# Optimization experiments

Measured on AMD Instinct MI355X. Metric: run time of the kernel, lower is better.

## Reference

```python
import jax, jax.numpy as jnp
import numpy as np

NUM_EMBEDDINGS = 4096
EMBED_DIM = 256
BETA = 0.25


def setup_inputs() -> dict:
    key = jax.random.key(0)
    kz, ke = jax.random.split(key)
    z = jax.random.normal(kz, (16, 4096, EMBED_DIM), dtype=jnp.float32)
    lim = 1.0 / NUM_EMBEDDINGS
    emb = jax.random.uniform(ke, (NUM_EMBEDDINGS, EMBED_DIM), dtype=jnp.float32,
                             minval=-lim, maxval=lim)
    return {"z": z, "emb": emb}


def reference(z, emb):
    B, T, D = z.shape
    flat_z = z.reshape(-1, D)                                  # [N, D]
    # squared euclidean distances via ||z||^2 - 2 z.e^T + ||e||^2
    dist = (jnp.sum(flat_z ** 2, axis=1, keepdims=True)
            - 2.0 * flat_z @ emb.T
            + jnp.sum(emb ** 2, axis=1))                       # [N, K]
    indices = jnp.argmin(dist, axis=1)                         # [N]
    z_q = emb[indices].reshape(z.shape)                        # [B, T, D]
    sg = jax.lax.stop_gradient
    codebook_loss = jnp.mean((sg(z_q) - z) ** 2)
    commit_loss = jnp.mean((z_q - sg(z)) ** 2)
    loss = codebook_loss + BETA * commit_loss
    z_q_st = z + sg(z_q - z)                                   # straight-through
    return z_q_st, loss, indices.reshape(B, T)
```

## Files before the change

### kernel.cpp

```cpp
#include <hip/hip_runtime.h>

#define N_ROWS 65536
#define K_CODES 4096
#define D_DIM 256
#define MARGIN_BF 6.0e-5f
#define CAP_DUEL 24576
#define CAP_FULL 8192

typedef __attribute__((ext_vector_type(8))) _Float16 f16x8;
typedef __attribute__((ext_vector_type(4))) float f32x4;

typedef __attribute__((address_space(1))) unsigned int g_u32;
typedef __attribute__((address_space(3))) unsigned int l_u32;
#define GLOAD16(gp, lp) __builtin_amdgcn_global_load_lds((g_u32*)(gp), (l_u32*)(lp), 16, 0, 0)


union f16u { _Float16 h; unsigned short u; };

static __device__ __forceinline__ unsigned int pack2(float a, float b) {
    f16u x, y; x.h = (_Float16)a; y.h = (_Float16)b;
    return (unsigned)x.u | ((unsigned)y.u << 16);
}

static __device__ __forceinline__ void norm_body(const float* __restrict__ src,
                                                 float* __restrict__ dst, int bi, int tid) {
    int row = bi * 64 + (tid >> 2);
    int q = tid & 3;
    const float* p = src + (size_t)row * D_DIM;
    double acc = 0.0;
#pragma unroll 4
    for (int it = 0; it < 16; ++it) {
        float4 v = *(const float4*)&p[(q + 4 * it) * 4];
        float a = v.x * v.x, b = v.y * v.y, c = v.z * v.z, d = v.w * v.w;
        acc += (double)a; acc += (double)b; acc += (double)c; acc += (double)d;
    }
    acc += __shfl_xor(acc, 1);
    acc += __shfl_xor(acc, 2);
    if (q == 0) dst[row] = (float)acc;
}

__global__ __launch_bounds__(256) void cvt_emb_kernel(const float* __restrict__ emb,
                                                      unsigned short* __restrict__ emb_perm,
                                                      float* __restrict__ cvec,
                                                      int* __restrict__ cnts,
                                                      unsigned long long* __restrict__ rescored) {
    if (blockIdx.x >= 512) {
        if (blockIdx.x == 512 && threadIdx.x < 2) cnts[threadIdx.x] = 0;
        norm_body(emb, cvec, blockIdx.x - 512, threadIdx.x);
        return;
    }
    if (blockIdx.x < 256) rescored[blockIdx.x * 256 + threadIdx.x] = ~0ull;
    int gid = blockIdx.x * 256 + threadIdx.x;
    int lane = gid & 63;
    int f = gid >> 6;
    int cf = f & 1;
    int d8 = (f >> 1) & 7;
    int step = (f >> 4) & 63;
    int h = f >> 10;
    int code = h * 2048 + step * 32 + cf * 16 + (lane & 15);
    int d0 = d8 * 32 + (lane >> 4) * 8;
    const float* p = emb + (size_t)code * D_DIM + d0;
    float4 v0 = *(const float4*)p;
    float4 v1 = *(const float4*)(p + 4);
    uint4 o;
    o.x = pack2(v0.x * 4096.0f, v0.y * 4096.0f);
    o.y = pack2(v0.z * 4096.0f, v0.w * 4096.0f);
    o.z = pack2(v1.x * 4096.0f, v1.y * 4096.0f);
    o.w = pack2(v1.z * 4096.0f, v1.w * 4096.0f);
    *(uint4*)((char*)emb_perm + (size_t)gid * 16) = o;
}

__global__ __launch_bounds__(256) void cvt_z_kernel(const float* __restrict__ z,
                                                    unsigned short* __restrict__ z_perm) {
    int ft = blockIdx.x * 256 + threadIdx.x;
    int lane = ft & 63;
    int rf = (ft >> 6) & 3;
    int d8 = (ft >> 8) & 7;
    int rg = ft >> 11;
    int row = rg * 64 + rf * 16 + (lane & 15);
    int d0 = d8 * 32 + (lane >> 4) * 8;
    const float* p = z + (size_t)row * D_DIM + d0;
    float4 v0 = *(const float4*)p;
    float4 v1 = *(const float4*)(p + 4);
    uint4 o;
    o.x = pack2(v0.x, v0.y);
    o.y = pack2(v0.z, v0.w);
    o.z = pack2(v1.x, v1.y);
    o.w = pack2(v1.z, v1.w);
    *(uint4*)((char*)z_perm + (size_t)ft * 16) = o;
}

__global__ __launch_bounds__(256, 2) void phaseB_kernel(
        const unsigned short* __restrict__ z_perm, const unsigned short* __restrict__ emb_perm,
        const float* __restrict__ cvec, float* __restrict__ out_idx,
        int* __restrict__ cnts, int* __restrict__ fulllist,
        unsigned long long* __restrict__ duellist) {
    __shared__ float cv[4096];
    __shared__ unsigned short ring[2][8][1024];

    const int tid = threadIdx.x;
    const int lane = tid & 63;
    const int w = tid >> 6;
    const int pp = w >> 1;
    const int h = w & 1;
    const int l15 = lane & 15, l4 = lane >> 4;
    const int rb = blockIdx.x;

#pragma unroll
    for (int i = 0; i < 4; ++i) {
        int idx = i * 1024 + tid * 4;
        *(float4*)&cv[idx] = *(const float4*)&cvec[idx];
    }

    f16x8 A[8][4];
    {
        const char* zsrc = (const char*)z_perm + (size_t)(rb * 2 + pp) * 32768 + lane * 16;
#pragma unroll
        for (int d8 = 0; d8 < 8; ++d8)
#pragma unroll
            for (int rf = 0; rf < 4; ++rf)
                A[d8][rf] = *(const f16x8*)(zsrc + (d8 * 4 + rf) * 1024);
    }
    __syncthreads();

    const char* bsrc = (const char*)emb_perm + (size_t)h * 1048576 + pp * 1024 + lane * 16;
    char* ldst = (char*)&ring[h][0][0] + pp * 1024;
    const char* lrd = (const char*)&ring[h][0][0] + lane * 16;

#pragma unroll
    for (int q = 0; q < 6; ++q)
        GLOAD16(bsrc + q * 2048, ldst + q * 2048);
    asm volatile("s_waitcnt vmcnt(5)" ::: "memory");
    __builtin_amdgcn_s_barrier();
    __builtin_amdgcn_sched_barrier(0);

    f16x8 B0a = *(const f16x8*)(lrd);
    f16x8 B0b = *(const f16x8*)(lrd + 1024);
    f16x8 B1a, B1b;

    float m1[16], m2[16], m3[16];
#pragma unroll
    for (int t = 0; t < 16; ++t) { m1[t] = 3.4e38f; m2[t] = 3.4e38f; m3[t] = 3.4e38f; }

    f32x4 acc[4][2];

    for (int step = 0; step < 64; ++step) {
        const int kb = h * 2048 + step * 32;
        float ck0 = cv[kb + l15];
        float ck1 = cv[kb + 16 + l15];
#pragma unroll
        for (int rf = 0; rf < 4; ++rf) {
            acc[rf][0] = (f32x4){0.f, 0.f, 0.f, 0.f};
            acc[rf][1] = (f32x4){0.f, 0.f, 0.f, 0.f};
        }
#pragma unroll
        for (int d8 = 0; d8 < 8; ++d8) {
            {
                const char* g = bsrc + (size_t)(step * 8 + d8 + 6) * 2048
                                - ((step == 63 && d8 >= 2) ? 1048576 : 0);
                GLOAD16(g, ldst + ((d8 + 6) & 7) * 2048);
            }
            asm volatile("s_waitcnt vmcnt(5)" ::: "memory");
            __builtin_amdgcn_s_barrier();
            __builtin_amdgcn_sched_barrier(0);
            {
                const char* rp = lrd + ((d8 + 1) & 7) * 2048;
                if ((d8 + 1) & 1) { B1a = *(const f16x8*)rp; B1b = *(const f16x8*)(rp + 1024); }
                else              { B0a = *(const f16x8*)rp; B0b = *(const f16x8*)(rp + 1024); }
            }
            f16x8 b0 = (d8 & 1) ? B1a : B0a;
            f16x8 b1 = (d8 & 1) ? B1b : B0b;
#pragma unroll
            for (int rf = 0; rf < 4; ++rf) {
                acc[rf][0] = __builtin_amdgcn_mfma_f32_16x16x32_f16(A[d8][rf], b0, acc[rf][0], 0, 0, 0);
                acc[rf][1] = __builtin_amdgcn_mfma_f32_16x16x32_f16(A[d8][rf], b1, acc[rf][1], 0, 0, 0);
            }
        }

#pragma unroll
        for (int cf = 0; cf < 2; ++cf) {
            const float ck = cf ? ck1 : ck0;
            const unsigned cg = (unsigned)(kb + cf * 16 + l15);
#pragma unroll
            for (int rf = 0; rf < 4; ++rf)
#pragma unroll
                for (int j = 0; j < 4; ++j) {
                    float d = fmaf(-4.8828125e-4f, acc[rf][cf][j], ck);
                    float dp = __uint_as_float((__float_as_uint(d) & 0xfffff000u) | cg);
                    const int t = rf * 4 + j;
                    m3[t] = __builtin_amdgcn_fmed3f(dp, m2[t], m3[t]);
                    m2[t] = __builtin_amdgcn_fmed3f(dp, m1[t], m2[t]);
                    m1[t] = fminf(m1[t], dp);
                }
        }
    }

    __syncthreads();
    float* m1s = cv;
    float* m2s = cv + 256;
    float* m3s = cv + 512;
#pragma unroll
    for (int t = 0; t < 16; ++t) {
        float a1 = m1[t], a2 = m2[t], a3 = m3[t];
        for (int msk = 8; msk >= 1; msk >>= 1) {
            float b1 = __shfl_xor(a1, msk);
            float b2 = __shfl_xor(a2, msk);
            float b3 = __shfl_xor(a3, msk);
            bool bw = b1 < a1;
            float w1 = bw ? b1 : a1, w2 = bw ? b2 : a2, w3 = bw ? b3 : a3;
            float l1 = bw ? a1 : b1, l2 = bw ? a2 : b2;
            bool t2 = l1 < w2;
            a1 = w1;
            a2 = t2 ? l1 : w2;
            a3 = t2 ? fminf(w2, l2) : fminf(w3, l1);
        }
        if (l15 == 0) {
            int rloc = (t >> 2) * 16 + l4 * 4 + (t & 3);
            m1s[w * 64 + rloc] = a1;
            m2s[w * 64 + rloc] = a2;
            m3s[w * 64 + rloc] = a3;
        }
    }
    __syncthreads();

    if (tid < 128) {
        int pg = tid >> 6, r = tid & 63;
        int wA = pg * 2, wB = pg * 2 + 1;
        float a1 = m1s[wA * 64 + r], a2 = m2s[wA * 64 + r], a3 = m3s[wA * 64 + r];
        float b1 = m1s[wB * 64 + r], b2 = m2s[wB * 64 + r], b3 = m3s[wB * 64 + r];
        bool bw = b1 < a1;
        float w1 = bw ? b1 : a1, w2 = bw ? b2 : a2, w3 = bw ? b3 : a3;
        float l1 = bw ? a1 : b1, l2 = bw ? a2 : b2;
        bool t2 = l1 < w2;
        float f1 = w1;
        float f2 = t2 ? l1 : w2;
        float f3 = t2 ? fminf(w2, l2) : fminf(w3, l1);

        int i1 = (int)(__float_as_uint(f1) & 0xfffu);
        int i2 = (int)(__float_as_uint(f2) & 0xfffu);
        int rowg = rb * 128 + pg * 64 + r;
        out_idx[rowg] = (float)i1;
        if (f3 - f1 < MARGIN_BF) {
            int pz = atomicAdd(&cnts[1], 1);
            if (pz < CAP_FULL) fulllist[pz] = rowg;
        } else if (f2 - f1 < MARGIN_BF) {
            int pz = atomicAdd(&cnts[0], 1);
            if (pz < CAP_DUEL) {
                duellist[pz] = ((unsigned long long)(unsigned)rowg << 32) |
                               ((unsigned)i1 << 16) | (unsigned)i2;
            } else {
                int pf = atomicAdd(&cnts[1], 1);
                if (pf < CAP_FULL) fulllist[pf] = rowg;
            }
        }
    }
}

__global__ __launch_bounds__(256) void duel_kernel(
        const float* __restrict__ z, const float* __restrict__ emb,
        const float* __restrict__ cvec,
        const int* __restrict__ cnts, const unsigned long long* __restrict__ duellist,
        unsigned long long* __restrict__ rescored) {
    int n = cnts[0];
    if (n > CAP_DUEL) n = CAP_DUEL;
    for (int i = blockIdx.x * 256 + threadIdx.x; i < n; i += 64 * 256) {
        unsigned long long e = duellist[i];
        int row = (int)(e >> 32);
        int c1 = (int)((e >> 16) & 0xfffu);
        int c2 = (int)(e & 0xfffu);
        const float* zp = z + (size_t)row * D_DIM;
        const float* p1 = emb + (size_t)c1 * D_DIM;
        const float* p2 = emb + (size_t)c2 * D_DIM;
        float a1 = 0.f, a2 = 0.f;
        double n0 = 0.0, n1 = 0.0, n2 = 0.0, n3 = 0.0;
#pragma unroll 8
        for (int d4 = 0; d4 < 64; ++d4) {
            float4 zf = *(const float4*)&zp[d4 * 4];
            float4 e1 = *(const float4*)&p1[d4 * 4];
            float4 e2 = *(const float4*)&p2[d4 * 4];
            a1 = fmaf(zf.x, e1.x, a1); a1 = fmaf(zf.y, e1.y, a1);
            a1 = fmaf(zf.z, e1.z, a1); a1 = fmaf(zf.w, e1.w, a1);
            a2 = fmaf(zf.x, e2.x, a2); a2 = fmaf(zf.y, e2.y, a2);
            a2 = fmaf(zf.z, e2.z, a2); a2 = fmaf(zf.w, e2.w, a2);
            float sx = zf.x * zf.x, sy = zf.y * zf.y, sz = zf.z * zf.z, sw = zf.w * zf.w;
            switch (d4 & 3) {
                case 0: n0 += (double)sx; n0 += (double)sy; n0 += (double)sz; n0 += (double)sw; break;
                case 1: n1 += (double)sx; n1 += (double)sy; n1 += (double)sz; n1 += (double)sw; break;
                case 2: n2 += (double)sx; n2 += (double)sy; n2 += (double)sz; n2 += (double)sw; break;
                default: n3 += (double)sx; n3 += (double)sy; n3 += (double)sz; n3 += (double)sw; break;
            }
        }
        float rn = (float)((n0 + n1) + (n2 + n3));
        float d1 = __fadd_rn(__fsub_rn(rn, __fmul_rn(2.0f, a1)), cvec[c1]);
        float d2 = __fadd_rn(__fsub_rn(rn, __fmul_rn(2.0f, a2)), cvec[c2]);
        unsigned long long p1v = ((unsigned long long)__float_as_uint(d1) << 32) | (unsigned)c1;
        unsigned long long p2v = ((unsigned long long)__float_as_uint(d2) << 32) | (unsigned)c2;
        rescored[row] = p1v < p2v ? p1v : p2v;
    }
}

__global__ __launch_bounds__(256) void rescore_kernel(
        const float* __restrict__ z, const float* __restrict__ emb,
        const float* __restrict__ cvec,
        const int* __restrict__ cnts, const int* __restrict__ fulllist,
        unsigned long long* __restrict__ rescored) {
    __shared__ float zs[16][256];
    __shared__ float sa[16];
    __shared__ int srow[16];
    const int tid = threadIdx.x;
    int cnt = cnts[1];
    if (cnt > CAP_FULL) cnt = CAP_FULL;
    const int nu = ((cnt + 15) >> 4) << 2;
    for (int uu = blockIdx.x; uu < nu; uu += gridDim.x) {
        int rg = uu >> 2, ks = uu & 3;
        __syncthreads();
        if (tid < 16) {
            int fi = rg * 16 + tid;
            srow[tid] = fulllist[fi < cnt ? fi : 0];
        }
        __syncthreads();
#pragma unroll
        for (int i = 0; i < 4; ++i) {
            int u = i * 256 + tid;
            int r = u >> 6, d4 = u & 63;
            *(float4*)&zs[r][d4 * 4] = *(const float4*)&z[(size_t)srow[r] * D_DIM + d4 * 4];
        }
        __syncthreads();
        if (tid < 64) {
            int r = tid >> 2, q = tid & 3;
            double acc = 0.0;
#pragma unroll 4
            for (int it = 0; it < 16; ++it) {
                float4 v = *(const float4*)&zs[r][(q + 4 * it) * 4];
                float a = v.x * v.x, b = v.y * v.y, c = v.z * v.z, d = v.w * v.w;
                acc += (double)a; acc += (double)b; acc += (double)c; acc += (double)d;
            }
            acc += __shfl_xor(acc, 1);
            acc += __shfl_xor(acc, 2);
            if (q == 0) sa[r] = (float)acc;
        }
        __syncthreads();

        const int c0 = ks * 1024 + tid;
        float acc[16][4];
#pragma unroll
        for (int r = 0; r < 16; ++r)
#pragma unroll
            for (int j = 0; j < 4; ++j) acc[r][j] = 0.f;

        for (int ch = 0; ch < 8; ++ch) {
#pragma unroll
            for (int q = 0; q < 8; ++q) {
                float4 e0 = *(const float4*)&emb[(size_t)(c0      ) * D_DIM + ch * 32 + q * 4];
                float4 e1 = *(const float4*)&emb[(size_t)(c0 + 256) * D_DIM + ch * 32 + q * 4];
                float4 e2 = *(const float4*)&emb[(size_t)(c0 + 512) * D_DIM + ch * 32 + q * 4];
                float4 e3 = *(const float4*)&emb[(size_t)(c0 + 768) * D_DIM + ch * 32 + q * 4];
#pragma unroll
                for (int r = 0; r < 16; ++r) {
                    float4 zf = *(const float4*)&zs[r][ch * 32 + q * 4];
                    acc[r][0] = fmaf(zf.x, e0.x, acc[r][0]);
                    acc[r][0] = fmaf(zf.y, e0.y, acc[r][0]);
                    acc[r][0] = fmaf(zf.z, e0.z, acc[r][0]);
                    acc[r][0] = fmaf(zf.w, e0.w, acc[r][0]);
                    acc[r][1] = fmaf(zf.x, e1.x, acc[r][1]);
                    acc[r][1] = fmaf(zf.y, e1.y, acc[r][1]);
                    acc[r][1] = fmaf(zf.z, e1.z, acc[r][1]);
                    acc[r][1] = fmaf(zf.w, e1.w, acc[r][1]);
                    acc[r][2] = fmaf(zf.x, e2.x, acc[r][2]);
                    acc[r][2] = fmaf(zf.y, e2.y, acc[r][2]);
                    acc[r][2] = fmaf(zf.z, e2.z, acc[r][2]);
                    acc[r][2] = fmaf(zf.w, e2.w, acc[r][2]);
                    acc[r][3] = fmaf(zf.x, e3.x, acc[r][3]);
                    acc[r][3] = fmaf(zf.y, e3.y, acc[r][3]);
                    acc[r][3] = fmaf(zf.z, e3.z, acc[r][3]);
                    acc[r][3] = fmaf(zf.w, e3.w, acc[r][3]);
                }
            }
        }
        const float ck0 = cvec[c0], ck1 = cvec[c0 + 256];
        const float ck2 = cvec[c0 + 512], ck3 = cvec[c0 + 768];
#pragma unroll
        for (int r = 0; r < 16; ++r) {
            float d0 = __fadd_rn(__fsub_rn(sa[r], __fmul_rn(2.0f, acc[r][0])), ck0);
            float d1 = __fadd_rn(__fsub_rn(sa[r], __fmul_rn(2.0f, acc[r][1])), ck1);
            float d2 = __fadd_rn(__fsub_rn(sa[r], __fmul_rn(2.0f, acc[r][2])), ck2);
            float d3 = __fadd_rn(__fsub_rn(sa[r], __fmul_rn(2.0f, acc[r][3])), ck3);
            unsigned long long p0 = ((unsigned long long)__float_as_uint(d0) << 32) | (unsigned)(c0);
            unsigned long long p1 = ((unsigned long long)__float_as_uint(d1) << 32) | (unsigned)(c0 + 256);
            unsigned long long p2 = ((unsigned long long)__float_as_uint(d2) << 32) | (unsigned)(c0 + 512);
            unsigned long long p3 = ((unsigned long long)__float_as_uint(d3) << 32) | (unsigned)(c0 + 768);
            unsigned long long pa = p0 < p1 ? p0 : p1;
            unsigned long long pb = p2 < p3 ? p2 : p3;
            unsigned long long pm = pa < pb ? pa : pb;
            for (int msk = 32; msk >= 1; msk >>= 1) {
                unsigned long long qv = __shfl_xor(pm, msk);
                pm = qv < pm ? qv : pm;
            }
            if ((tid & 63) == 0) atomicMin(&rescored[srow[r]], pm);
        }
    }
}

__global__ __launch_bounds__(256) void writeback_kernel(
        const float* __restrict__ z, const float* __restrict__ emb,
        const unsigned long long* __restrict__ rescored,
        float* __restrict__ out_idx, float* __restrict__ out0,
        double* __restrict__ partials) {
    const int tid = threadIdx.x;
    const int base = blockIdx.x * 32;
    double acc = 0.0;
    for (int g = 0; g < 8; ++g) {
        int row = base + g * 4 + (tid >> 6);
        int d4 = tid & 63;
        unsigned long long rv = rescored[row];
        int idx;
        if (rv != ~0ull) {
            idx = (int)(unsigned)(rv & 0xffffffffull);
            if (d4 == 0) out_idx[row] = (float)idx;
        } else {
            idx = (int)out_idx[row];
        }
        float4 q4 = *(const float4*)&emb[(size_t)idx * D_DIM + d4 * 4];
        float4 z4 = *(const float4*)&z[(size_t)row * D_DIM + d4 * 4];
        float4 o;
        float dx;
        dx = q4.x - z4.x; o.x = z4.x + dx; acc += (double)dx * dx;
        dx = q4.y - z4.y; o.y = z4.y + dx; acc += (double)dx * dx;
        dx = q4.z - z4.z; o.z = z4.z + dx; acc += (double)dx * dx;
        dx = q4.w - z4.w; o.w = z4.w + dx; acc += (double)dx * dx;
        *(float4*)&out0[(size_t)row * D_DIM + d4 * 4] = o;
    }
    for (int m = 32; m >= 1; m >>= 1) acc += __shfl_xor(acc, m);
    __shared__ double sd[4];
    if ((tid & 63) == 0) sd[tid >> 6] = acc;
    __syncthreads();
    if (tid == 0) partials[blockIdx.x] = (sd[0] + sd[1]) + (sd[2] + sd[3]);
}

__global__ void finalize_kernel(const double* __restrict__ partials, float* __restrict__ out_loss) {
    __shared__ double sd[256];
    const int tid = threadIdx.x;
    double a = 0.0;
    for (int i = tid; i < 2048; i += 256) a += partials[i];
    sd[tid] = a;
    __syncthreads();
    for (int s = 128; s > 0; s >>= 1) {
        if (tid < s) sd[tid] += sd[tid + s];
        __syncthreads();
    }
    if (tid == 0) {
        double m = sd[0] / 16777216.0;
        out_loss[0] = (float)(m + 0.25 * m);
    }
}

extern "C" void kernel_launch(void* const* d_in, const int* in_sizes, int n_in,
                              void* d_out, int out_size, void* d_ws, size_t ws_size,
                              hipStream_t stream) {
    const float* z = (const float*)d_in[0];
    const float* emb = (const float*)d_in[1];
    float* out0 = (float*)d_out;
    float* out_loss = out0 + (size_t)N_ROWS * D_DIM;
    float* out_idx = out_loss + 1;

    char* ws = (char*)d_ws;
    float* cvec = (float*)(ws + 262144);
    unsigned short* emb_perm = (unsigned short*)(ws + 278528);
    int* cnts = (int*)(ws + 2375680);
    int* fulllist = (int*)(ws + 2375936);
    unsigned long long* duellist = (unsigned long long*)(ws + 2408704);
    unsigned long long* rescored = (unsigned long long*)(ws + 2605312);
    double* partials = (double*)(ws + 3129600);

    unsigned short* z_perm = (unsigned short*)d_out;

    cvt_emb_kernel<<<576, 256, 0, stream>>>(emb, emb_perm, cvec, cnts, rescored);
    cvt_z_kernel<<<8192, 256, 0, stream>>>(z, z_perm);
    phaseB_kernel<<<512, 256, 0, stream>>>(z_perm, emb_perm, cvec, out_idx, cnts, fulllist, duellist);
    rescore_kernel<<<256, 256, 0, stream>>>(z, emb, cvec, cnts, fulllist, rescored);
    duel_kernel<<<64, 256, 0, stream>>>(z, emb, cvec, cnts, duellist, rescored);
    writeback_kernel<<<N_ROWS / 32, 256, 0, stream>>>(z, emb, rescored, out_idx, out0, partials);
    finalize_kernel<<<1, 256, 0, stream>>>(partials, out_loss);
}
```

Baseline: 286.7 us.

## Merge conversion and refinement kernels; batch writeback loads over more blocks

Fuses the z and codebook conversion kernels into one launch, and runs the full-rescore and duel-rescore paths as disjoint block ranges of a single refine kernel, so they overlap and inter-kernel gaps shrink. The writeback kernel now handles 16 rows per block instead of 32, with the index lookups and loads hoisted ahead of the compute to expose memory parallelism. The finalize step reads twice as many partials. The cost is a larger partials buffer and more heterogeneous blocks within each kernel.

```diff
diff --git a/kernel.cpp b/kernel.cpp
--- a/kernel.cpp
+++ b/kernel.cpp
@@ -39,55 +39,56 @@
     if (q == 0) dst[row] = (float)acc;
 }
 
-__global__ __launch_bounds__(256) void cvt_emb_kernel(const float* __restrict__ emb,
+__global__ __launch_bounds__(256) void cvt_all_kernel(const float* __restrict__ z,
+                                                      const float* __restrict__ emb,
+                                                      unsigned short* __restrict__ z_perm,
                                                       unsigned short* __restrict__ emb_perm,
                                                       float* __restrict__ cvec,
                                                       int* __restrict__ cnts,
                                                       unsigned long long* __restrict__ rescored) {
-    if (blockIdx.x >= 512) {
-        if (blockIdx.x == 512 && threadIdx.x < 2) cnts[threadIdx.x] = 0;
-        norm_body(emb, cvec, blockIdx.x - 512, threadIdx.x);
-        return;
-    }
-    if (blockIdx.x < 256) rescored[blockIdx.x * 256 + threadIdx.x] = ~0ull;
-    int gid = blockIdx.x * 256 + threadIdx.x;
-    int lane = gid & 63;
-    int f = gid >> 6;
-    int cf = f & 1;
-    int d8 = (f >> 1) & 7;
-    int step = (f >> 4) & 63;
-    int h = f >> 10;
-    int code = h * 2048 + step * 32 + cf * 16 + (lane & 15);
-    int d0 = d8 * 32 + (lane >> 4) * 8;
-    const float* p = emb + (size_t)code * D_DIM + d0;
-    float4 v0 = *(const float4*)p;
-    float4 v1 = *(const float4*)(p + 4);
-    uint4 o;
-    o.x = pack2(v0.x * 4096.0f, v0.y * 4096.0f);
-    o.y = pack2(v0.z * 4096.0f, v0.w * 4096.0f);
-    o.z = pack2(v1.x * 4096.0f, v1.y * 4096.0f);
-    o.w = pack2(v1.z * 4096.0f, v1.w * 4096.0f);
-    *(uint4*)((char*)emb_perm + (size_t)gid * 16) = o;
-}
-
-__global__ __launch_bounds__(256) void cvt_z_kernel(const float* __restrict__ z,
-                                                    unsigned short* __restrict__ z_perm) {
-    int ft = blockIdx.x * 256 + threadIdx.x;
-    int lane = ft & 63;
-    int rf = (ft >> 6) & 3;
-    int d8 = (ft >> 8) & 7;
-    int rg = ft >> 11;
-    int row = rg * 64 + rf * 16 + (lane & 15);
-    int d0 = d8 * 32 + (lane >> 4) * 8;
-    const float* p = z + (size_t)row * D_DIM + d0;
-    float4 v0 = *(const float4*)p;
-    float4 v1 = *(const float4*)(p + 4);
-    uint4 o;
-    o.x = pack2(v0.x, v0.y);
-    o.y = pack2(v0.z, v0.w);
-    o.z = pack2(v1.x, v1.y);
-    o.w = pack2(v1.z, v1.w);
-    *(uint4*)((char*)z_perm + (size_t)ft * 16) = o;
+    const int b = blockIdx.x;
+    const int tid = threadIdx.x;
+    if (b < 8192) {
+        if (b < 256) rescored[b * 256 + tid] = ~0ull;
+        int ft = b * 256 + tid;
+        int lane = ft & 63;
+        int rf = (ft >> 6) & 3;
+        int d8 = (ft >> 8) & 7;
+        int rg = ft >> 11;
+        int row = rg * 64 + rf * 16 + (lane & 15);
+        int d0 = d8 * 32 + (lane >> 4) * 8;
+        const float* p = z + (size_t)row * D_DIM + d0;
+        float4 v0 = *(const float4*)p;
+        float4 v1 = *(const float4*)(p + 4);
+        uint4 o;
+        o.x = pack2(v0.x, v0.y);
+        o.y = pack2(v0.z, v0.w);
+        o.z = pack2(v1.x, v1.y);
+        o.w = pack2(v1.z, v1.w);
+        *(uint4*)((char*)z_perm + (size_t)ft * 16) = o;
+    } else if (b < 8704) {
+        int gid = (b - 8192) * 256 + tid;
+        int lane = gid & 63;
+        int f = gid >> 6;
+        int cf = f & 1;
+        int d8 = (f >> 1) & 7;
+        int step = (f >> 4) & 63;
+        int h = f >> 10;
+        int code = h * 2048 + step * 32 + cf * 16 + (lane & 15);
+        int d0 = d8 * 32 + (lane >> 4) * 8;
+        const float* p = emb + (size_t)code * D_DIM + d0;
+        float4 v0 = *(const float4*)p;
+        float4 v1 = *(const float4*)(p + 4);
+        uint4 o;
+        o.x = pack2(v0.x * 4096.0f, v0.y * 4096.0f);
+        o.y = pack2(v0.z * 4096.0f, v0.w * 4096.0f);
+        o.z = pack2(v1.x * 4096.0f, v1.y * 4096.0f);
+        o.w = pack2(v1.z * 4096.0f, v1.w * 4096.0f);
+        *(uint4*)((char*)emb_perm + (size_t)gid * 16) = o;
+    } else {
+        if (b == 8704 && tid < 2) cnts[tid] = 0;
+        norm_body(emb, cvec, b - 8704, tid);
+    }
 }
 
 __global__ __launch_bounds__(256, 2) void phaseB_kernel(
@@ -256,62 +257,61 @@
     }
 }
 
-__global__ __launch_bounds__(256) void duel_kernel(
-        const float* __restrict__ z, const float* __restrict__ emb,
-        const float* __restrict__ cvec,
-        const int* __restrict__ cnts, const unsigned long long* __restrict__ duellist,
-        unsigned long long* __restrict__ rescored) {
-    int n = cnts[0];
-    if (n > CAP_DUEL) n = CAP_DUEL;
-    for (int i = blockIdx.x * 256 + threadIdx.x; i < n; i += 64 * 256) {
-        unsigned long long e = duellist[i];
-        int row = (int)(e >> 32);
-        int c1 = (int)((e >> 16) & 0xfffu);
-        int c2 = (int)(e & 0xfffu);
-        const float* zp = z + (size_t)row * D_DIM;
-        const float* p1 = emb + (size_t)c1 * D_DIM;
-        const float* p2 = emb + (size_t)c2 * D_DIM;
-        float a1 = 0.f, a2 = 0.f;
-        double n0 = 0.0, n1 = 0.0, n2 = 0.0, n3 = 0.0;
-#pragma unroll 8
-        for (int d4 = 0; d4 < 64; ++d4) {
-            float4 zf = *(const float4*)&zp[d4 * 4];
-            float4 e1 = *(const float4*)&p1[d4 * 4];
-            float4 e2 = *(const float4*)&p2[d4 * 4];
-            a1 = fmaf(zf.x, e1.x, a1); a1 = fmaf(zf.y, e1.y, a1);
-            a1 = fmaf(zf.z, e1.z, a1); a1 = fmaf(zf.w, e1.w, a1);
-            a2 = fmaf(zf.x, e2.x, a2); a2 = fmaf(zf.y, e2.y, a2);
-            a2 = fmaf(zf.z, e2.z, a2); a2 = fmaf(zf.w, e2.w, a2);
-            float sx = zf.x * zf.x, sy = zf.y * zf.y, sz = zf.z * zf.z, sw = zf.w * zf.w;
-            switch (d4 & 3) {
-                case 0: n0 += (double)sx; n0 += (double)sy; n0 += (double)sz; n0 += (double)sw; break;
-                case 1: n1 += (double)sx; n1 += (double)sy; n1 += (double)sz; n1 += (double)sw; break;
-                case 2: n2 += (double)sx; n2 += (double)sy; n2 += (double)sz; n2 += (double)sw; break;
-                default: n3 += (double)sx; n3 += (double)sy; n3 += (double)sz; n3 += (double)sw; break;
-            }
-        }
-        float rn = (float)((n0 + n1) + (n2 + n3));
-        float d1 = __fadd_rn(__fsub_rn(rn, __fmul_rn(2.0f, a1)), cvec[c1]);
-        float d2 = __fadd_rn(__fsub_rn(rn, __fmul_rn(2.0f, a2)), cvec[c2]);
-        unsigned long long p1v = ((unsigned long long)__float_as_uint(d1) << 32) | (unsigned)c1;
-        unsigned long long p2v = ((unsigned long long)__float_as_uint(d2) << 32) | (unsigned)c2;
-        rescored[row] = p1v < p2v ? p1v : p2v;
-    }
-}
-
-__global__ __launch_bounds__(256) void rescore_kernel(
+__global__ __launch_bounds__(256) void refine_kernel(
         const float* __restrict__ z, const float* __restrict__ emb,
         const float* __restrict__ cvec,
         const int* __restrict__ cnts, const int* __restrict__ fulllist,
+        const unsigned long long* __restrict__ duellist,
         unsigned long long* __restrict__ rescored) {
     __shared__ float zs[16][256];
     __shared__ float sa[16];
     __shared__ int srow[16];
     const int tid = threadIdx.x;
+
+    if (blockIdx.x >= 256) {
+        int n = cnts[0];
+        if (n > CAP_DUEL) n = CAP_DUEL;
+        for (int i = (blockIdx.x - 256) * 256 + tid; i < n; i += 64 * 256) {
+            unsigned long long e = duellist[i];
+            int row = (int)(e >> 32);
+            int c1 = (int)((e >> 16) & 0xfffu);
+            int c2 = (int)(e & 0xfffu);
+            const float* zp = z + (size_t)row * D_DIM;
+            const float* p1 = emb + (size_t)c1 * D_DIM;
+            const float* p2 = emb + (size_t)c2 * D_DIM;
+            float a1 = 0.f, a2 = 0.f;
+            double n0 = 0.0, n1 = 0.0, n2 = 0.0, n3 = 0.0;
+#pragma unroll 8
+            for (int d4 = 0; d4 < 64; ++d4) {
+                float4 zf = *(const float4*)&zp[d4 * 4];
+                float4 e1 = *(const float4*)&p1[d4 * 4];
+                float4 e2 = *(const float4*)&p2[d4 * 4];
+                a1 = fmaf(zf.x, e1.x, a1); a1 = fmaf(zf.y, e1.y, a1);
+                a1 = fmaf(zf.z, e1.z, a1); a1 = fmaf(zf.w, e1.w, a1);
+                a2 = fmaf(zf.x, e2.x, a2); a2 = fmaf(zf.y, e2.y, a2);
+                a2 = fmaf(zf.z, e2.z, a2); a2 = fmaf(zf.w, e2.w, a2);
+                float sx = zf.x * zf.x, sy = zf.y * zf.y, sz = zf.z * zf.z, sw = zf.w * zf.w;
+                switch (d4 & 3) {
+                    case 0: n0 += (double)sx; n0 += (double)sy; n0 += (double)sz; n0 += (double)sw; break;
+                    case 1: n1 += (double)sx; n1 += (double)sy; n1 += (double)sz; n1 += (double)sw; break;
+                    case 2: n2 += (double)sx; n2 += (double)sy; n2 += (double)sz; n2 += (double)sw; break;
+                    default: n3 += (double)sx; n3 += (double)sy; n3 += (double)sz; n3 += (double)sw; break;
+                }
+            }
+            float rn = (float)((n0 + n1) + (n2 + n3));
+            float d1 = __fadd_rn(__fsub_rn(rn, __fmul_rn(2.0f, a1)), cvec[c1]);
+            float d2 = __fadd_rn(__fsub_rn(rn, __fmul_rn(2.0f, a2)), cvec[c2]);
+            unsigned long long p1v = ((unsigned long long)__float_as_uint(d1) << 32) | (unsigned)c1;
+            unsigned long long p2v = ((unsigned long long)__float_as_uint(d2) << 32) | (unsigned)c2;
+            rescored[row] = p1v < p2v ? p1v : p2v;
+        }
+        return;
+    }
+
     int cnt = cnts[1];
     if (cnt > CAP_FULL) cnt = CAP_FULL;
     const int nu = ((cnt + 15) >> 4) << 2;
-    for (int uu = blockIdx.x; uu < nu; uu += gridDim.x) {
+    for (int uu = blockIdx.x; uu < nu; uu += 256) {
         int rg = uu >> 2, ks = uu & 3;
         __syncthreads();
         if (tid < 16) {
@@ -407,28 +407,36 @@
         float* __restrict__ out_idx, float* __restrict__ out0,
         double* __restrict__ partials) {
     const int tid = threadIdx.x;
-    const int base = blockIdx.x * 32;
+    const int base = blockIdx.x * 16;
+    const int d4 = tid & 63;
+    int rows[4], idx[4];
+    unsigned long long rv[4];
+#pragma unroll
+    for (int g = 0; g < 4; ++g) {
+        rows[g] = base + g * 4 + (tid >> 6);
+        rv[g] = rescored[rows[g]];
+    }
+#pragma unroll
+    for (int g = 0; g < 4; ++g) {
+        if (rv[g] != ~0ull) {
+            idx[g] = (int)(unsigned)(rv[g] & 0xffffffffull);
+            if (d4 == 0) out_idx[rows[g]] = (float)idx[g];
+        } else {
+            idx[g] = (int)out_idx[rows[g]];
+        }
+    }
     double acc = 0.0;
-    for (int g = 0; g < 8; ++g) {
-        int row = base + g * 4 + (tid >> 6);
-        int d4 = tid & 63;
-        unsigned long long rv = rescored[row];
-        int idx;
-        if (rv != ~0ull) {
-            idx = (int)(unsigned)(rv & 0xffffffffull);
-            if (d4 == 0) out_idx[row] = (float)idx;
-        } else {
-            idx = (int)out_idx[row];
-        }
-        float4 q4 = *(const float4*)&emb[(size_t)idx * D_DIM + d4 * 4];
-        float4 z4 = *(const float4*)&z[(size_t)row * D_DIM + d4 * 4];
+#pragma unroll
+    for (int g = 0; g < 4; ++g) {
+        float4 q4 = *(const float4*)&emb[(size_t)idx[g] * D_DIM + d4 * 4];
+        float4 z4 = *(const float4*)&z[(size_t)rows[g] * D_DIM + d4 * 4];
         float4 o;
         float dx;
         dx = q4.x - z4.x; o.x = z4.x + dx; acc += (double)dx * dx;
         dx = q4.y - z4.y; o.y = z4.y + dx; acc += (double)dx * dx;
         dx = q4.z - z4.z; o.z = z4.z + dx; acc += (double)dx * dx;
         dx = q4.w - z4.w; o.w = z4.w + dx; acc += (double)dx * dx;
-        *(float4*)&out0[(size_t)row * D_DIM + d4 * 4] = o;
+        *(float4*)&out0[(size_t)rows[g] * D_DIM + d4 * 4] = o;
     }
     for (int m = 32; m >= 1; m >>= 1) acc += __shfl_xor(acc, m);
     __shared__ double sd[4];
@@ -441,7 +449,7 @@
     __shared__ double sd[256];
     const int tid = threadIdx.x;
     double a = 0.0;
-    for (int i = tid; i < 2048; i += 256) a += partials[i];
+    for (int i = tid; i < 4096; i += 256) a += partials[i];
     sd[tid] = a;
     __syncthreads();
     for (int s = 128; s > 0; s >>= 1) {
@@ -474,11 +482,9 @@
 
     unsigned short* z_perm = (unsigned short*)d_out;
 
-    cvt_emb_kernel<<<576, 256, 0, stream>>>(emb, emb_perm, cvec, cnts, rescored);
-    cvt_z_kernel<<<8192, 256, 0, stream>>>(z, z_perm);
+    cvt_all_kernel<<<8768, 256, 0, stream>>>(z, emb, z_perm, emb_perm, cvec, cnts, rescored);
     phaseB_kernel<<<512, 256, 0, stream>>>(z_perm, emb_perm, cvec, out_idx, cnts, fulllist, duellist);
-    rescore_kernel<<<256, 256, 0, stream>>>(z, emb, cvec, cnts, fulllist, rescored);
-    duel_kernel<<<64, 256, 0, stream>>>(z, emb, cvec, cnts, duellist, rescored);
-    writeback_kernel<<<N_ROWS / 32, 256, 0, stream>>>(z, emb, rescored, out_idx, out0, partials);
+    refine_kernel<<<320, 256, 0, stream>>>(z, emb, cvec, cnts, fulllist, duellist, rescored);
+    writeback_kernel<<<N_ROWS / 16, 256, 0, stream>>>(z, emb, rescored, out_idx, out0, partials);
     finalize_kernel<<<1, 256, 0, stream>>>(partials, out_loss);
 }
```

After: 279.1 us. 2.7% less time.
